# Performance work log

Measured on AMD Instinct MI355X. Metric: run time of the kernel, lower is better.

## Reference

```python
import jax, jax.numpy as jnp
import numpy as np

H = 64      # hidden_size
FQ = 32     # freq_size
IN = 16     # input_size
BSZ = 32    # batch
ROW = 32
COL = 32


def setup_inputs() -> dict:
    key = jax.random.key(0)
    ks = jax.random.split(key, 14)
    stdv = 1.0 / np.sqrt(H)
    u = lambda k, shape: jax.random.uniform(k, shape, jnp.float32, -stdv, stdv)
    return {
        "x": jax.random.normal(ks[0], (BSZ, ROW, COL, IN), jnp.float32),
        "W_first": u(ks[1], (6 * H, IN + 2 * H)),
        "W_freq": u(ks[2], (2 * FQ, IN + 2 * H)),
        "B_gate": u(ks[3], (1, 6 * H)),
        "B_freq": u(ks[4], (1, 2 * FQ)),
        "row_c_w": u(ks[5], (1, FQ)),
        "row_c_b": u(ks[6], (1,)),
        "col_c_w": u(ks[7], (1, FQ)),
        "col_c_b": u(ks[8], (1,)),
        "row_o_w": u(ks[9], (H, H)),
        "row_o_b": u(ks[10], (H,)),
        "col_o_w": u(ks[11], (H, H)),
        "col_o_b": u(ks[12], (H,)),
    }


def _forward(x, W_first, W_freq, B_gate, B_freq, row_c_w, row_c_b,
             col_c_w, col_c_b, row_o_w, row_o_b, col_o_w, col_o_b):
    Bsz, R, C, I = x.shape
    # col <= row path of the torch code: permute(1,0,2,3)
    xin = jnp.transpose(x, (1, 0, 2, 3))          # [SN, B, OSL, I]
    SN, OSL = R, C                                 # Water2sea_slice_num, Original_slice_len
    L = SN + OSL - 1                               # Water2sea_slice_len
    NB = SN * Bsz
    Hh = row_o_w.shape[0]
    Fq = row_c_w.shape[1]
    omega = 2.0 * jnp.pi * jnp.arange(1, Fq + 1, dtype=jnp.float32) / Fq  # [Fq]

    # Build diagonal-shifted input_transfer without loops
    r_idx = jnp.arange(SN)
    t_idx = jnp.arange(L)
    rel = t_idx[None, :] - r_idx[:, None]          # [SN, L]
    valid = (rel >= 0) & (rel < OSL)
    rel_c = jnp.clip(rel, 0, OSL - 1)
    a_full = jnp.take_along_axis(xin, rel_c[:, None, :, None], axis=2)  # [SN,B,L,I]
    a_full = jnp.where(valid[:, None, :, None], a_full, 0.0)
    a_seq = a_full.reshape(NB, L, I).transpose(1, 0, 2)                  # [L,NB,I]

    # time tensor; torch rolls it by Bsz each step, so precompute cur_time per step
    time_mat = jnp.where(valid, (r_idx[:, None] * OSL + rel).astype(jnp.float32), 0.0)  # [SN,L]
    time_orig = jnp.broadcast_to(time_mat[:, None, :], (SN, Bsz, L)).reshape(NB, L)
    i_idx = (jnp.arange(NB)[None, :] - t_idx[:, None] * Bsz) % NB        # roll by s*Bsz
    cur_time = time_orig[i_idx, t_idx[:, None]]                          # [L,NB]
    cos_all = jnp.cos(cur_time[:, :, None] * omega)                      # [L,NB,Fq]
    sin_all = jnp.sin(cur_time[:, :, None] * omega)

    # bias mask: bias added only to first B*(s+1) rows, and only if s < SN
    bmask = ((t_idx[:, None] < SN) &
             (jnp.arange(NB)[None, :] < Bsz * (t_idx[:, None] + 1))).astype(jnp.float32)  # [L,NB]

    B0, Bf0 = B_gate[0], B_freq[0]

    def step(carry, inp):
        h_row, h_col, rr, ri, cr, ci, s = carry
        a_s, cos_s, sin_s, bm = inp
        xcat = jnp.concatenate([h_row, h_col, a_s], axis=-1)            # [NB, 2H+I]
        gate = xcat @ W_first.T + bm[:, None] * B0                      # [NB, 6H]
        fg = jax.nn.sigmoid(xcat @ W_freq.T + bm[:, None] * Bf0)        # [NB, 2F]
        row_freq, col_freq = fg[:, :Fq], fg[:, Fq:]
        sg = jax.nn.sigmoid(gate[:, :4 * Hh])
        tg = jnp.tanh(gate[:, 4 * Hh:])
        ig_row, ig_col = tg[:, :Hh], tg[:, Hh:]
        ug_row, og_row = sg[:, :Hh], sg[:, Hh:2 * Hh]
        ug_col, og_col = sg[:, 2 * Hh:3 * Hh], sg[:, 3 * Hh:]
        row_ft = ug_row[:, :, None] * row_freq[:, None, :]              # [NB,H,F]
        col_ft = ug_col[:, :, None] * col_freq[:, None, :]
        amp_r = (og_row * ig_row)[:, :, None]
        amp_c = (og_col * ig_col)[:, :, None]
        rr = row_ft * rr + amp_r * cos_s[:, None, :]
        ri = row_ft * ri + amp_r * sin_s[:, None, :]
        cr = col_ft * cr + amp_c * cos_s[:, None, :]
        ci = col_ft * ci + amp_c * sin_s[:, None, :]
        row_c = jnp.tanh((rr * rr + ri * ri) @ row_c_w[0] + row_c_b[0])  # [NB,H]
        col_c = jnp.tanh((cr * cr + ci * ci) @ col_c_w[0] + col_c_b[0])
        h_row = jax.nn.sigmoid((1.0 - ug_row) * h_row + ug_row * ig_row
                               + row_c @ row_o_w.T + row_o_b) * row_c
        h_col = jax.nn.sigmoid((1.0 - ug_col) * h_col + ug_col * ig_col
                               + col_c @ col_o_w.T + col_o_b) * col_c
        out_slice = jnp.concatenate([h_row, h_col], axis=-1)            # [NB,2H]
        start = jnp.clip((s - OSL + 1) * Bsz, 0, NB - Bsz)
        row_chunk = jax.lax.dynamic_slice(h_row, (start, 0), (Bsz, Hh))
        col_chunk = h_col[(SN - 1) * Bsz:]
        h_col_r = jnp.roll(h_col, Bsz, axis=0)
        cr_r = jnp.roll(cr, Bsz, axis=0)
        ci_r = jnp.roll(ci, Bsz, axis=0)
        return (h_row, h_col_r, rr, ri, cr_r, ci_r, s + 1), (out_slice, row_chunk, col_chunk)

    ones_hf = 0.1 * jnp.ones((NB, Hh, Fq), jnp.float32)
    init = (jnp.zeros((NB, Hh), jnp.float32), jnp.zeros((NB, Hh), jnp.float32),
            ones_hf, ones_hf, ones_hf, ones_hf, jnp.int32(0))
    _, (outs, rows, cols) = jax.lax.scan(step, init, (a_seq, cos_all, sin_all, bmask))
    output_all = outs.transpose(1, 0, 2)                                # [NB,L,2H]
    hidden_row_all = rows[OSL - 1:].transpose(1, 0, 2).reshape(Bsz, 1, SN, Hh)
    hidden_col_all = cols[SN - 1:].transpose(1, 0, 2).reshape(Bsz, 1, OSL, Hh)
    return output_all, hidden_row_all, hidden_col_all


def reference(x, W_first, W_freq, B_gate, B_freq, row_c_w, row_c_b,
              col_c_w, col_c_b, row_o_w, row_o_b, col_o_w, col_o_b):
    return _forward(x, W_first, W_freq, B_gate, B_freq, row_c_w, row_c_b,
                    col_c_w, col_c_b, row_o_w, row_o_b, col_o_w, col_o_b)
```

## Files before the change

### kernel.cpp

```cpp
#include <hip/hip_runtime.h>
#include <math.h>

#define HN   64
#define SNN  32
#define OSLN 32
#define LTN  63
#define KXN  144

#define OUT_HR 8257536
#define OUT_HC 8323072

#define WS_HROW 0
#define WS_HCOL 262144
#define WS_COS  524288
#define WS_SIN  557056
#define WS_FLG  589824

struct KParams {
  const float *x, *Wf, *Wq, *Bg, *Bq, *rcw, *rcb, *ccw, *ccb, *r_ow, *r_ob, *c_ow, *c_ob;
  float *ws;
  float *out;
};

__device__ __forceinline__ float bcast(float v, int k) {
  return __int_as_float(__builtin_amdgcn_readlane(__float_as_int(v), k));
}

__device__ __forceinline__ float sigm_fast(float x) {
  return __builtin_amdgcn_rcpf(1.0f + __expf(-x));
}
__device__ __forceinline__ float tanh_fast(float x) {
  float a = fabsf(x);
  float e = __expf(-2.0f * a);
  float r = (1.0f - e) * __builtin_amdgcn_rcpf(1.0f + e);
  return copysignf(r, x);
}

__device__ __forceinline__ float coh_load(const float* p) {
  return __uint_as_float(__hip_atomic_load((unsigned*)p, __ATOMIC_RELAXED, __HIP_MEMORY_SCOPE_AGENT));
}
__device__ __forceinline__ void coh_store(float* p, float v) {
  __hip_atomic_store((unsigned*)p, __float_as_uint(v), __ATOMIC_RELAXED, __HIP_MEMORY_SCOPE_AGENT);
}
__device__ __forceinline__ unsigned flag_load(const unsigned* p) {
  return __hip_atomic_load((unsigned*)p, __ATOMIC_RELAXED, __HIP_MEMORY_SCOPE_AGENT);
}
__device__ __forceinline__ void flag_store(unsigned* p, unsigned v) {
  __hip_atomic_store(p, v, __ATOMIC_RELAXED, __HIP_MEMORY_SCOPE_AGENT);
}
__device__ __forceinline__ unsigned* flg(float* ws, int b, int side, int grp) {
  return (unsigned*)(ws + WS_FLG) + ((((b << 1) | side) << 3) + grp) * 32;
}

__global__ void init_kernel(float* ws) {
  size_t i0 = (size_t)blockIdx.x * blockDim.x + threadIdx.x;
  size_t stride = (size_t)gridDim.x * blockDim.x;
  for (size_t i = i0; i < 524288; i += stride) ws[i] = 0.0f;
  for (size_t i = i0; i < 32768; i += stride) {
    int ct = (int)(i >> 5);
    int f  = (int)(i & 31);
    float om = (6.2831853071795862f * (float)(f + 1)) * 0.03125f;
    float th = (float)ct * om;
    ws[WS_COS + i] = cosf(th);
    ws[WS_SIN + i] = sinf(th);
  }
  for (size_t i = i0; i < 16384; i += stride)
    ((unsigned*)(ws + WS_FLG))[i] = 0u;
}

#define GATE_BATCH8(XC, W4, K0)                                          \
  {                                                                      \
    float t00 = bcast(XC[0], (K0)),     t01 = bcast(XC[1], (K0));        \
    float t02 = bcast(XC[2], (K0)),     t03 = bcast(XC[3], (K0));        \
    float t10 = bcast(XC[0], (K0) + 1), t11 = bcast(XC[1], (K0) + 1);    \
    float t12 = bcast(XC[2], (K0) + 1), t13 = bcast(XC[3], (K0) + 1);    \
    acc[0] = fmaf(W4.x, t00, acc[0]); acc[1] = fmaf(W4.x, t01, acc[1]);  \
    acc[2] = fmaf(W4.x, t02, acc[2]); acc[3] = fmaf(W4.x, t03, acc[3]);  \
    acc[0] = fmaf(W4.y, t10, acc[0]); acc[1] = fmaf(W4.y, t11, acc[1]);  \
    acc[2] = fmaf(W4.y, t12, acc[2]); acc[3] = fmaf(W4.y, t13, acc[3]);  \
    float u00 = bcast(XC[0], (K0) + 2), u01 = bcast(XC[1], (K0) + 2);    \
    float u02 = bcast(XC[2], (K0) + 2), u03 = bcast(XC[3], (K0) + 2);    \
    float u10 = bcast(XC[0], (K0) + 3), u11 = bcast(XC[1], (K0) + 3);    \
    float u12 = bcast(XC[2], (K0) + 3), u13 = bcast(XC[3], (K0) + 3);    \
    acc[0] = fmaf(W4.z, u00, acc[0]); acc[1] = fmaf(W4.z, u01, acc[1]);  \
    acc[2] = fmaf(W4.z, u02, acc[2]); acc[3] = fmaf(W4.z, u03, acc[3]);  \
    acc[0] = fmaf(W4.w, u10, acc[0]); acc[1] = fmaf(W4.w, u11, acc[1]);  \
    acc[2] = fmaf(W4.w, u12, acc[2]); acc[3] = fmaf(W4.w, u13, acc[3]);  \
  }

__global__ __launch_bounds__(256, 2) void fused_kernel(KParams p) {
  __shared__ float gl[4][224];
  __shared__ float hown[4][64];
  __shared__ float cvec[4][64];

  const int blk = blockIdx.x;
  const int b   = blk & 31;
  const int sub = blk >> 5;
  const bool isRow = (sub < 8);
  const int g   = sub & 7;
  const int c0  = g << 2;
  const int tid = threadIdx.x;
  const int lane = tid & 63;
  const int hh = tid >> 2, f0 = (tid & 3) << 3;
  const int hp = tid & 63, mg = tid >> 6;

  const int side  = isRow ? 0 : 1;
  unsigned* fOwn  = flg(p.ws, b, side, g);

  const int j = (tid < 224) ? tid : 223;
  const float* Wrow; float bias;
  if (j < 192) {
    int jr = isRow ? ((j < 128) ? j : j + 128)
                   : ((j < 128) ? j + 128 : j + 192);
    Wrow = p.Wf + jr * KXN; bias = p.Bg[jr];
  } else {
    int jf = isRow ? (j - 192) : (j - 160);
    Wrow = p.Wq + jf * KXN; bias = p.Bq[jf];
  }
  float wfv[8];
  { const float* w = isRow ? p.rcw : p.ccw;
#pragma unroll
    for (int fi = 0; fi < 8; ++fi) wfv[fi] = w[f0 + fi]; }
  const float cbv = isRow ? p.rcb[0] : p.ccb[0];
  const float ob  = (isRow ? p.r_ob : p.c_ob)[hp];
  const float* OW = (isRow ? p.r_ow : p.c_ow) + hp * HN;

  float rr[4][8], ri[4][8];
#pragma unroll
  for (int i = 0; i < 4; ++i)
#pragma unroll
    for (int fi = 0; fi < 8; ++fi) { rr[i][fi] = 0.1f; ri[i][fi] = 0.1f; }

  hown[mg][hp] = 0.0f;
  __syncthreads();

  for (int t = 0; t < LTN; ++t) {
    if (t > 0) {
      if (tid == 0) {
        int a = isRow ? ((c0 - t) & 31) : ((c0 + t) & 31);
        unsigned* f1 = flg(p.ws, b, 1 - side, a >> 2);
        unsigned* f2 = flg(p.ws, b, 1 - side, ((a + 3) & 31) >> 2);
        const unsigned need = (unsigned)t;
        int guard = 0;
        while ((flag_load(f1) < need || flag_load(f2) < need) && ++guard < 4000000)
          __builtin_amdgcn_s_sleep(1);
      }
      __syncthreads();
    }

    int r8[4], cc8[4];
#pragma unroll
    for (int i = 0; i < 4; ++i) {
      int ch = c0 + i;
      r8[i]  = isRow ? ch : ((ch + t) & 31);
      cc8[i] = isRow ? ((ch - t) & 31) : ch;
    }
    const float* hrowR = p.ws + WS_HROW + (size_t)(t & 3) * 65536;
    float*       hrowW = p.ws + WS_HROW + (size_t)((t + 1) & 3) * 65536;
    const float* hcolR = p.ws + WS_HCOL + (size_t)(t & 3) * 65536;
    float*       hcolW = p.ws + WS_HCOL + (size_t)((t + 1) & 3) * 65536;

    float xc0[4], xc1[4], xc2[4];
#pragma unroll
    for (int i = 0; i < 4; ++i) {
      int r = r8[i], cc = cc8[i];
      int cdx = t - r;
      bool av = (cdx >= 0) && (cdx < OSLN);
      if (isRow) {
        xc0[i] = hown[i][lane];
        xc1[i] = coh_load(&hcolR[(((cc << 5) | b) << 6) + lane]);
      } else {
        xc1[i] = hown[i][lane];
        xc0[i] = coh_load(&hrowR[(((r << 5) | b) << 6) + lane]);
      }
      xc2[i] = (av && lane < 16) ? p.x[(size_t)((((b << 5) | r) << 5) | cdx) * 16 + lane] : 0.0f;
    }
    float acc[4] = {0.f,0.f,0.f,0.f};
    for (int kb = 0; kb < 64; kb += 4) {
      float4 w4 = *(const float4*)(Wrow + kb);
      GATE_BATCH8(xc0, w4, kb);
    }
    for (int kb = 64; kb < 128; kb += 4) {
      float4 w4 = *(const float4*)(Wrow + kb);
      GATE_BATCH8(xc1, w4, kb - 64);
    }
#pragma unroll
    for (int kb = 128; kb < 144; kb += 4) {
      float4 w4 = *(const float4*)(Wrow + kb);
      GATE_BATCH8(xc2, w4, kb - 128);
    }
    if (tid < 224) {
      const bool isT = (tid >= 128 && tid < 192);
#pragma unroll
      for (int i = 0; i < 4; ++i) {
        float bm = (t < SNN && r8[i] <= t) ? 1.0f : 0.0f;
        float v = fmaf(bm, bias, acc[i]);
        gl[i][tid] = isT ? tanh_fast(v) : sigm_fast(v);
      }
    }
    __syncthreads();

#pragma unroll
    for (int i = 0; i < 4; ++i) {
      int cc = cc8[i];
      int tcd = t - cc;
      int ctI = (tcd >= 0 && tcd < OSLN) ? ((cc << 5) + tcd) : 0;
      const float* cp = p.ws + WS_COS + (ctI << 5) + f0;
      const float* sp = p.ws + WS_SIN + (ctI << 5) + f0;
      float csv[8], snv[8];
      *(float4*)(csv)     = *(const float4*)(cp);
      *(float4*)(csv + 4) = *(const float4*)(cp + 4);
      *(float4*)(snv)     = *(const float4*)(sp);
      *(float4*)(snv + 4) = *(const float4*)(sp + 4);
      float ug = gl[i][hh];
      float og = gl[i][64 + hh];
      float ig = gl[i][128 + hh];
      float amp = og * ig;
      float fr[8];
      *(float4*)(fr)     = *(const float4*)(&gl[i][192 + f0]);
      *(float4*)(fr + 4) = *(const float4*)(&gl[i][192 + f0 + 4]);
      float sq = 0.0f;
#pragma unroll
      for (int fi = 0; fi < 8; ++fi) {
        float ft = ug * fr[fi];
        rr[i][fi] = fmaf(ft, rr[i][fi], amp * csv[fi]);
        ri[i][fi] = fmaf(ft, ri[i][fi], amp * snv[fi]);
        sq = fmaf(fmaf(ri[i][fi], ri[i][fi], rr[i][fi] * rr[i][fi]), wfv[fi], sq);
      }
      sq += __shfl_xor(sq, 1);
      sq += __shfl_xor(sq, 2);
      if ((tid & 3) == 0) cvec[i][hh] = tanh_fast(sq + cbv);
    }
    __syncthreads();

    float u0 = 0.0f;
    for (int k = 0; k < 64; k += 4) {
      float4 w4 = *(const float4*)(OW + k);
      u0 = fmaf(w4.x, cvec[mg][k],     u0);
      u0 = fmaf(w4.y, cvec[mg][k + 1], u0);
      u0 = fmaf(w4.z, cvec[mg][k + 2], u0);
      u0 = fmaf(w4.w, cvec[mg][k + 3], u0);
    }
    {
      const int i = mg;
      float ug = gl[i][hp];
      float ig = gl[i][128 + hp];
      float hOld = hown[i][hp];
      float cval = cvec[i][hp];
      float pre = (1.0f - ug) * hOld + ug * ig + u0 + ob;
      float hn = sigm_fast(pre) * cval;
      hown[i][hp] = hn;
      int r = r8[i], cc = cc8[i];
      int n = (r << 5) | b;
      if (isRow) {
        coh_store(&hrowW[(n << 6) + hp], hn);
        p.out[(((size_t)n * LTN) + t) * 128 + hp] = hn;
        if (t >= 31 && r == t - 31)
          p.out[OUT_HR + (((b << 5) | r) << 6) + hp] = hn;
      } else {
        coh_store(&hcolW[(((cc << 5) | b) << 6) + hp], hn);
        p.out[(((size_t)n * LTN) + t) * 128 + 64 + hp] = hn;
        if (t >= 31 && r == 31)
          p.out[OUT_HC + (((b << 5) | (t - 31)) << 6) + hp] = hn;
      }
    }

    if (t < LTN - 1) {
      __syncthreads();
      if (tid == 0) flag_store(fOwn, (unsigned)(t + 1));
    }
  }
}

extern "C" void kernel_launch(void* const* d_in, const int* in_sizes, int n_in,
                              void* d_out, int out_size, void* d_ws, size_t ws_size,
                              hipStream_t stream) {
  KParams p;
  p.x    = (const float*)d_in[0];
  p.Wf   = (const float*)d_in[1];
  p.Wq   = (const float*)d_in[2];
  p.Bg   = (const float*)d_in[3];
  p.Bq   = (const float*)d_in[4];
  p.rcw  = (const float*)d_in[5];
  p.rcb  = (const float*)d_in[6];
  p.ccw  = (const float*)d_in[7];
  p.ccb  = (const float*)d_in[8];
  p.r_ow = (const float*)d_in[9];
  p.r_ob = (const float*)d_in[10];
  p.c_ow = (const float*)d_in[11];
  p.c_ob = (const float*)d_in[12];
  p.ws   = (float*)d_ws;
  p.out  = (float*)d_out;

  hipLaunchKernelGGL(init_kernel, dim3(256), dim3(256), 0, stream, p.ws);
  hipLaunchKernelGGL(fused_kernel, dim3(512), dim3(256), 0, stream, p);
}
```

Before: 792.7 us.

## Split work across twice as many blocks with two chains per block

Each block now handles two row/column chains instead of four, doubling the grid to 1024 blocks and raising launch bounds to four blocks per CU. The flag array and group indexing are resized to match the finer decomposition. The aim is to spread the serial per-timestep recurrence over more CUs and cut per-block latency per step. In exchange there are more inter-block flag waits, more redundant weight loads per block, and the last phase leaves half the threads idle.

```diff
diff --git a/kernel.cpp b/kernel.cpp
--- a/kernel.cpp
+++ b/kernel.cpp
@@ -49,7 +49,7 @@
   __hip_atomic_store(p, v, __ATOMIC_RELAXED, __HIP_MEMORY_SCOPE_AGENT);
 }
 __device__ __forceinline__ unsigned* flg(float* ws, int b, int side, int grp) {
-  return (unsigned*)(ws + WS_FLG) + ((((b << 1) | side) << 3) + grp) * 32;
+  return (unsigned*)(ws + WS_FLG) + ((((b << 1) | side) << 4) + grp) * 32;
 }
 
 __global__ void init_kernel(float* ws) {
@@ -64,41 +64,33 @@
     ws[WS_COS + i] = cosf(th);
     ws[WS_SIN + i] = sinf(th);
   }
-  for (size_t i = i0; i < 16384; i += stride)
+  for (size_t i = i0; i < 32768; i += stride)
     ((unsigned*)(ws + WS_FLG))[i] = 0u;
 }
 
-#define GATE_BATCH8(XC, W4, K0)                                          \
+#define GATE_BATCH4(XC, W4, K0)                                          \
   {                                                                      \
     float t00 = bcast(XC[0], (K0)),     t01 = bcast(XC[1], (K0));        \
-    float t02 = bcast(XC[2], (K0)),     t03 = bcast(XC[3], (K0));        \
     float t10 = bcast(XC[0], (K0) + 1), t11 = bcast(XC[1], (K0) + 1);    \
-    float t12 = bcast(XC[2], (K0) + 1), t13 = bcast(XC[3], (K0) + 1);    \
     acc[0] = fmaf(W4.x, t00, acc[0]); acc[1] = fmaf(W4.x, t01, acc[1]);  \
-    acc[2] = fmaf(W4.x, t02, acc[2]); acc[3] = fmaf(W4.x, t03, acc[3]);  \
     acc[0] = fmaf(W4.y, t10, acc[0]); acc[1] = fmaf(W4.y, t11, acc[1]);  \
-    acc[2] = fmaf(W4.y, t12, acc[2]); acc[3] = fmaf(W4.y, t13, acc[3]);  \
     float u00 = bcast(XC[0], (K0) + 2), u01 = bcast(XC[1], (K0) + 2);    \
-    float u02 = bcast(XC[2], (K0) + 2), u03 = bcast(XC[3], (K0) + 2);    \
     float u10 = bcast(XC[0], (K0) + 3), u11 = bcast(XC[1], (K0) + 3);    \
-    float u12 = bcast(XC[2], (K0) + 3), u13 = bcast(XC[3], (K0) + 3);    \
     acc[0] = fmaf(W4.z, u00, acc[0]); acc[1] = fmaf(W4.z, u01, acc[1]);  \
-    acc[2] = fmaf(W4.z, u02, acc[2]); acc[3] = fmaf(W4.z, u03, acc[3]);  \
     acc[0] = fmaf(W4.w, u10, acc[0]); acc[1] = fmaf(W4.w, u11, acc[1]);  \
-    acc[2] = fmaf(W4.w, u12, acc[2]); acc[3] = fmaf(W4.w, u13, acc[3]);  \
-  }
-
-__global__ __launch_bounds__(256, 2) void fused_kernel(KParams p) {
-  __shared__ float gl[4][224];
-  __shared__ float hown[4][64];
-  __shared__ float cvec[4][64];
+  }
+
+__global__ __launch_bounds__(256, 4) void fused_kernel(KParams p) {
+  __shared__ float gl[2][224];
+  __shared__ float hown[2][64];
+  __shared__ float cvec[2][64];
 
   const int blk = blockIdx.x;
   const int b   = blk & 31;
   const int sub = blk >> 5;
-  const bool isRow = (sub < 8);
-  const int g   = sub & 7;
-  const int c0  = g << 2;
+  const bool isRow = (sub < 16);
+  const int g   = sub & 15;
+  const int c0  = g << 1;
   const int tid = threadIdx.x;
   const int lane = tid & 63;
   const int hh = tid >> 2, f0 = (tid & 3) << 3;
@@ -125,21 +117,21 @@
   const float ob  = (isRow ? p.r_ob : p.c_ob)[hp];
   const float* OW = (isRow ? p.r_ow : p.c_ow) + hp * HN;
 
-  float rr[4][8], ri[4][8];
-#pragma unroll
-  for (int i = 0; i < 4; ++i)
+  float rr[2][8], ri[2][8];
+#pragma unroll
+  for (int i = 0; i < 2; ++i)
 #pragma unroll
     for (int fi = 0; fi < 8; ++fi) { rr[i][fi] = 0.1f; ri[i][fi] = 0.1f; }
 
-  hown[mg][hp] = 0.0f;
+  if (tid < 128) hown[tid >> 6][tid & 63] = 0.0f;
   __syncthreads();
 
   for (int t = 0; t < LTN; ++t) {
     if (t > 0) {
       if (tid == 0) {
         int a = isRow ? ((c0 - t) & 31) : ((c0 + t) & 31);
-        unsigned* f1 = flg(p.ws, b, 1 - side, a >> 2);
-        unsigned* f2 = flg(p.ws, b, 1 - side, ((a + 3) & 31) >> 2);
+        unsigned* f1 = flg(p.ws, b, 1 - side, a >> 1);
+        unsigned* f2 = flg(p.ws, b, 1 - side, ((a + 1) & 31) >> 1);
         const unsigned need = (unsigned)t;
         int guard = 0;
         while ((flag_load(f1) < need || flag_load(f2) < need) && ++guard < 4000000)
@@ -148,9 +140,9 @@
       __syncthreads();
     }
 
-    int r8[4], cc8[4];
-#pragma unroll
-    for (int i = 0; i < 4; ++i) {
+    int r8[2], cc8[2];
+#pragma unroll
+    for (int i = 0; i < 2; ++i) {
       int ch = c0 + i;
       r8[i]  = isRow ? ch : ((ch + t) & 31);
       cc8[i] = isRow ? ((ch - t) & 31) : ch;
@@ -160,9 +152,9 @@
     const float* hcolR = p.ws + WS_HCOL + (size_t)(t & 3) * 65536;
     float*       hcolW = p.ws + WS_HCOL + (size_t)((t + 1) & 3) * 65536;
 
-    float xc0[4], xc1[4], xc2[4];
-#pragma unroll
-    for (int i = 0; i < 4; ++i) {
+    float xc0[2], xc1[2], xc2[2];
+#pragma unroll
+    for (int i = 0; i < 2; ++i) {
       int r = r8[i], cc = cc8[i];
       int cdx = t - r;
       bool av = (cdx >= 0) && (cdx < OSLN);
@@ -175,24 +167,24 @@
       }
       xc2[i] = (av && lane < 16) ? p.x[(size_t)((((b << 5) | r) << 5) | cdx) * 16 + lane] : 0.0f;
     }
-    float acc[4] = {0.f,0.f,0.f,0.f};
+    float acc[2] = {0.f, 0.f};
     for (int kb = 0; kb < 64; kb += 4) {
       float4 w4 = *(const float4*)(Wrow + kb);
-      GATE_BATCH8(xc0, w4, kb);
+      GATE_BATCH4(xc0, w4, kb);
     }
     for (int kb = 64; kb < 128; kb += 4) {
       float4 w4 = *(const float4*)(Wrow + kb);
-      GATE_BATCH8(xc1, w4, kb - 64);
+      GATE_BATCH4(xc1, w4, kb - 64);
     }
 #pragma unroll
     for (int kb = 128; kb < 144; kb += 4) {
       float4 w4 = *(const float4*)(Wrow + kb);
-      GATE_BATCH8(xc2, w4, kb - 128);
+      GATE_BATCH4(xc2, w4, kb - 128);
     }
     if (tid < 224) {
       const bool isT = (tid >= 128 && tid < 192);
 #pragma unroll
-      for (int i = 0; i < 4; ++i) {
+      for (int i = 0; i < 2; ++i) {
         float bm = (t < SNN && r8[i] <= t) ? 1.0f : 0.0f;
         float v = fmaf(bm, bias, acc[i]);
         gl[i][tid] = isT ? tanh_fast(v) : sigm_fast(v);
@@ -201,7 +193,7 @@
     __syncthreads();
 
 #pragma unroll
-    for (int i = 0; i < 4; ++i) {
+    for (int i = 0; i < 2; ++i) {
       int cc = cc8[i];
       int tcd = t - cc;
       int ctI = (tcd >= 0 && tcd < OSLN) ? ((cc << 5) + tcd) : 0;
@@ -233,16 +225,16 @@
     }
     __syncthreads();
 
-    float u0 = 0.0f;
-    for (int k = 0; k < 64; k += 4) {
-      float4 w4 = *(const float4*)(OW + k);
-      u0 = fmaf(w4.x, cvec[mg][k],     u0);
-      u0 = fmaf(w4.y, cvec[mg][k + 1], u0);
-      u0 = fmaf(w4.z, cvec[mg][k + 2], u0);
-      u0 = fmaf(w4.w, cvec[mg][k + 3], u0);
-    }
-    {
+    if (mg < 2) {
       const int i = mg;
+      float u0 = 0.0f;
+      for (int k = 0; k < 64; k += 4) {
+        float4 w4 = *(const float4*)(OW + k);
+        u0 = fmaf(w4.x, cvec[i][k],     u0);
+        u0 = fmaf(w4.y, cvec[i][k + 1], u0);
+        u0 = fmaf(w4.z, cvec[i][k + 2], u0);
+        u0 = fmaf(w4.w, cvec[i][k + 3], u0);
+      }
       float ug = gl[i][hp];
       float ig = gl[i][128 + hp];
       float hOld = hown[i][hp];
@@ -293,5 +285,5 @@
   p.out  = (float*)d_out;
 
   hipLaunchKernelGGL(init_kernel, dim3(256), dim3(256), 0, stream, p.ws);
-  hipLaunchKernelGGL(fused_kernel, dim3(512), dim3(256), 0, stream, p);
-}
+  hipLaunchKernelGGL(fused_kernel, dim3(1024), dim3(256), 0, stream, p);
+}
```

After: 874.0 us. +10.2%, slower.
